# Kernel tuning notes

Hardware: AMD Instinct MI355X
Metric: run time of the kernel (lower is better)

## Reference

```python
import jax, jax.numpy as jnp
import numpy as np

N, L, D = 512, 40, 128      # batch, peptide length, embedding dim
O, K, MHC = 256, 9, 34      # out_channels, kernel_size, mhc_len
STRIDE = 1


def setup_inputs() -> dict:
    key = jax.random.key(0)
    k1, k2, k3 = jax.random.split(key, 3)
    peptide_x = jax.random.normal(k1, (N, L, D), dtype=jnp.float32)
    mhc_x = jax.random.normal(k2, (N, MHC, D), dtype=jnp.float32)
    weight = jax.random.normal(k3, (O, K, MHC), dtype=jnp.float32) * 0.02  # truncated_normal std=0.02 approx
    bias = jnp.zeros((O,), dtype=jnp.float32)
    return {"peptide_x": peptide_x, "mhc_x": mhc_x, "weight": weight, "bias": bias}


def reference(peptide_x, mhc_x, weight, bias):
    # Per-sample dynamic kernel generation: [n, O, d, K]
    kernel = jax.nn.relu(jnp.einsum('nld,okl->nodk', mhc_x, weight))
    k = weight.shape[1]
    T = (peptide_x.shape[1] - k) // STRIDE + 1  # conv1d output length
    # Sliding windows of the peptide: [n, T, K, d]
    idx = jnp.arange(T)[:, None] * STRIDE + jnp.arange(k)[None, :]
    win = peptide_x[:, idx, :]
    # Grouped (groups=batch) conv1d as a batched contraction: [n, O, T]
    out = jnp.einsum('ntkd,nodk->not', win, kernel) + bias[None, :, None]
    return out
```

## Files before the change

kernel.cpp:

```cpp
#include <hip/hip_runtime.h>
#include <hip/hip_bf16.h>

typedef unsigned short u16;
typedef unsigned int u32;
typedef __bf16 bf16x8 __attribute__((ext_vector_type(8)));
typedef float f32x4 __attribute__((ext_vector_type(4)));
typedef unsigned int u32x4 __attribute__((ext_vector_type(4)));
typedef unsigned int u32x2 __attribute__((ext_vector_type(2)));

#define NN 512
#define LL 40
#define DD 128
#define OO 256
#define KK 9
#define MHCL 34
#define TT 32
#define PSTR 136
#define KDSTR 72
#define WPADL 64

#define PEPT_U16 (LL * PSTR)
#define KS_U16   (32 * KDSTR)

__device__ __forceinline__ u16 f2bf(float x) {
    unsigned int u = __builtin_bit_cast(unsigned int, x);
    u = (u + 0x7FFFu + ((u >> 16) & 1u)) >> 16;
    return (u16)u;
}
__device__ __forceinline__ u32 pk2(float a, float b) {
    __hip_bfloat162 h = __float22bfloat162_rn(make_float2(a, b));
    u32 r;
    __builtin_memcpy(&r, &h, 4);
    return r;
}
__device__ __forceinline__ bf16x8 lds_read8(const u16* p) {
    u32x4 r;
    __builtin_memcpy(&r, __builtin_assume_aligned(p, 16), 16);
    return __builtin_bit_cast(bf16x8, r);
}
__device__ __forceinline__ f32x4 mfma16(bf16x8 a, bf16x8 b, f32x4 c) {
    return __builtin_amdgcn_mfma_f32_16x16x32_bf16(a, b, c, 0, 0, 0);
}

__global__ void w_convert(const float* __restrict__ wgt, u32* __restrict__ wp) {
    int i = blockIdx.x * 256 + threadIdx.x;
    if (i >= OO * KK * (WPADL / 2)) return;
    int o = i / (KK * (WPADL / 2));
    int r = i - o * (KK * (WPADL / 2));
    int k = r >> 5;
    int lp = (r & 31) << 1;
    const float* src = wgt + ((size_t)o * KK + k) * MHCL;
    float a = (lp     < MHCL) ? src[lp]     : 0.f;
    float b = (lp + 1 < MHCL) ? src[lp + 1] : 0.f;
    wp[i] = pk2(a, b);
}

template<bool PRE>
__global__ __launch_bounds__(256, 2)
void iconv_kernel(const float* __restrict__ pept,
                  const float* __restrict__ mhc,
                  const float* __restrict__ wgt,
                  const u16* __restrict__ wp,
                  const float* __restrict__ bias,
                  float* __restrict__ out)
{
    __shared__ __align__(16) u16 s_mem[PEPT_U16 + 4 * KS_U16];

    const int tid  = threadIdx.x;
    const int wave = tid >> 6;
    const int pair = wave >> 1;
    const int dh   = wave & 1;
    const int lane = tid & 63;
    const int quad = lane >> 4;
    const int l16  = lane & 15;

    const int n  = blockIdx.x >> 2;
    const int oq = blockIdx.x & 3;
    const int obase = (oq * 2 + pair) * 32;

    u16* const s_pept = s_mem;
    u16* const ks     = s_mem + PEPT_U16 + wave * KS_U16;

    auto loadW = [&](int o_base, int k, bf16x8 wF[2][2]) {
        if (PRE) {
            #pragma unroll
            for (int mt = 0; mt < 2; ++mt) {
                const u16* wr = wp + ((size_t)(o_base + mt * 16 + l16) * KK + k) * WPADL;
                u32x4 r0, r1;
                __builtin_memcpy(&r0, __builtin_assume_aligned(wr + quad * 8, 16), 16);
                __builtin_memcpy(&r1, __builtin_assume_aligned(wr + 32 + quad * 8, 16), 16);
                wF[mt][0] = __builtin_bit_cast(bf16x8, r0);
                wF[mt][1] = __builtin_bit_cast(bf16x8, r1);
            }
        } else {
            #pragma unroll
            for (int mt = 0; mt < 2; ++mt) {
                const float* wrow = wgt + ((size_t)(o_base + mt * 16 + l16) * KK + k) * MHCL;
                float w8[8];
                __builtin_memcpy(w8, __builtin_assume_aligned(wrow + quad * 8, 8), 32);
                u16 h0[8];
                #pragma unroll
                for (int j = 0; j < 8; ++j) h0[j] = f2bf(w8[j]);
                __builtin_memcpy(&wF[mt][0], h0, 16);
                u16 h1[8] = {0,0,0,0,0,0,0,0};
                if (quad == 0) { h1[0] = f2bf(wrow[32]); h1[1] = f2bf(wrow[33]); }
                __builtin_memcpy(&wF[mt][1], h1, 16);
            }
        }
    };

    bf16x8 wB[2][2];
    loadW(obase, 0, wB);

    bf16x8 mA[4][2];
    {
        const float* mg = mhc + (size_t)n * MHCL * DD;
        #pragma unroll
        for (int di = 0; di < 4; ++di) {
            const int d = dh * 64 + di * 16 + l16;
            u16 h0[8];
            #pragma unroll
            for (int j = 0; j < 8; ++j)
                h0[j] = f2bf(mg[(size_t)(quad * 8 + j) * DD + d]);
            __builtin_memcpy(&mA[di][0], h0, 16);
            u16 h1[8] = {0,0,0,0,0,0,0,0};
            if (quad == 0) {
                h1[0] = f2bf(mg[(size_t)32 * DD + d]);
                h1[1] = f2bf(mg[(size_t)33 * DD + d]);
            }
            __builtin_memcpy(&mA[di][1], h1, 16);
        }
    }

    {
        const float* pg = pept + (size_t)n * LL * DD;
        #pragma unroll 1
        for (int i = tid; i < (LL * DD) / 4; i += 256) {
            int row = i >> 5, c4 = (i & 31) << 2;
            f32x4 v;
            __builtin_memcpy(&v, __builtin_assume_aligned(pg + row * DD + c4, 16), 16);
            u32x2 h = { pk2(v[0], v[1]), pk2(v[2], v[3]) };
            __builtin_memcpy(__builtin_assume_aligned(&s_pept[row * PSTR + c4], 8), &h, 8);
        }
    }
    __syncthreads();

    f32x4 acc00 = {0.f,0.f,0.f,0.f}, acc01 = acc00, acc10 = acc00, acc11 = acc00;

    #pragma unroll 3
    for (int k = 0; k < KK; ++k) {
        #pragma unroll
        for (int di = 0; di < 4; ++di) {
            f32x4 c0 = {0.f,0.f,0.f,0.f}, c1 = c0;
            c0 = mfma16(mA[di][0], wB[0][0], c0);
            c0 = mfma16(mA[di][1], wB[0][1], c0);
            c1 = mfma16(mA[di][0], wB[1][0], c1);
            c1 = mfma16(mA[di][1], wB[1][1], c1);
            u32x2 p0 = { pk2(fmaxf(c0[0], 0.f), fmaxf(c0[1], 0.f)),
                         pk2(fmaxf(c0[2], 0.f), fmaxf(c0[3], 0.f)) };
            u32x2 p1 = { pk2(fmaxf(c1[0], 0.f), fmaxf(c1[1], 0.f)),
                         pk2(fmaxf(c1[2], 0.f), fmaxf(c1[3], 0.f)) };
            __builtin_memcpy(__builtin_assume_aligned(&ks[l16 * KDSTR + di * 16 + quad * 4], 8), &p0, 8);
            __builtin_memcpy(__builtin_assume_aligned(&ks[(16 + l16) * KDSTR + di * 16 + quad * 4], 8), &p1, 8);
        }
        if (k < KK - 1) loadW(obase, k + 1, wB);
        #pragma unroll
        for (int ds = 0; ds < 2; ++ds) {
            bf16x8 kb0 = lds_read8(&ks[l16 * KDSTR + ds * 32 + quad * 8]);
            bf16x8 kb1 = lds_read8(&ks[(16 + l16) * KDSTR + ds * 32 + quad * 8]);
            bf16x8 ap0 = lds_read8(&s_pept[(k + l16) * PSTR + dh * 64 + ds * 32 + quad * 8]);
            bf16x8 ap1 = lds_read8(&s_pept[(k + 16 + l16) * PSTR + dh * 64 + ds * 32 + quad * 8]);
            acc00 = mfma16(ap0, kb0, acc00);
            acc01 = mfma16(ap0, kb1, acc01);
            acc10 = mfma16(ap1, kb0, acc10);
            acc11 = mfma16(ap1, kb1, acc11);
        }
    }

    if (dh == 1) {
        float* ox = (float*)ks;
        const int fb = lane * 16;
        __builtin_memcpy(__builtin_assume_aligned(&ox[fb +  0], 16), &acc00, 16);
        __builtin_memcpy(__builtin_assume_aligned(&ox[fb +  4], 16), &acc01, 16);
        __builtin_memcpy(__builtin_assume_aligned(&ox[fb +  8], 16), &acc10, 16);
        __builtin_memcpy(__builtin_assume_aligned(&ox[fb + 12], 16), &acc11, 16);
    }
    __syncthreads();
    if (dh == 0) {
        const float* px = (const float*)(s_mem + PEPT_U16 + (wave + 1) * KS_U16);
        const int fb = lane * 16;
        f32x4 q00, q01, q10, q11;
        __builtin_memcpy(&q00, __builtin_assume_aligned(&px[fb +  0], 16), 16);
        __builtin_memcpy(&q01, __builtin_assume_aligned(&px[fb +  4], 16), 16);
        __builtin_memcpy(&q10, __builtin_assume_aligned(&px[fb +  8], 16), 16);
        __builtin_memcpy(&q11, __builtin_assume_aligned(&px[fb + 12], 16), 16);
        const float bv0 = bias[obase + l16];
        const float bv1 = bias[obase + 16 + l16];
        f32x4 r00 = acc00 + q00 + bv0;
        f32x4 r01 = acc01 + q01 + bv1;
        f32x4 r10 = acc10 + q10 + bv0;
        f32x4 r11 = acc11 + q11 + bv1;
        float* ob = out + ((size_t)n * OO + obase) * TT;
        __builtin_memcpy(__builtin_assume_aligned(ob + (size_t)l16 * TT + quad * 4, 16), &r00, 16);
        __builtin_memcpy(__builtin_assume_aligned(ob + (size_t)(16 + l16) * TT + quad * 4, 16), &r01, 16);
        __builtin_memcpy(__builtin_assume_aligned(ob + (size_t)l16 * TT + 16 + quad * 4, 16), &r10, 16);
        __builtin_memcpy(__builtin_assume_aligned(ob + (size_t)(16 + l16) * TT + 16 + quad * 4, 16), &r11, 16);
    }
}

extern "C" void kernel_launch(void* const* d_in, const int* in_sizes, int n_in,
                              void* d_out, int out_size, void* d_ws, size_t ws_size,
                              hipStream_t stream) {
    const float* pept = (const float*)d_in[0];
    const float* mhc  = (const float*)d_in[1];
    const float* wgt  = (const float*)d_in[2];
    const float* bias = (const float*)d_in[3];
    float* out = (float*)d_out;

    const size_t w_bytes = (size_t)OO * KK * WPADL * sizeof(u16);
    if (ws_size >= w_bytes) {
        w_convert<<<dim3((OO * KK * (WPADL / 2) + 255) / 256), dim3(256), 0, stream>>>(wgt, (u32*)d_ws);
        iconv_kernel<true><<<dim3(NN * 4), dim3(256), 0, stream>>>(pept, mhc, wgt, (const u16*)d_ws, bias, out);
    } else {
        iconv_kernel<false><<<dim3(NN * 4), dim3(256), 0, stream>>>(pept, mhc, wgt, nullptr, bias, out);
    }
}
```

Before: 116.6 us.

## Pre-convert peptide to bf16 in workspace and read it directly from global

Adds a separate kernel that converts the whole peptide tensor to bf16 in the workspace. The main kernel then reads peptide fragments straight from global memory instead of staging them in LDS. This drops the peptide LDS buffer and the __syncthreads before the main loop, shrinking shared memory so the launch bound can rise to 6 blocks per CU. In exchange it adds an extra kernel launch and a full pass over the peptide. The main loop also now issues global loads, whose latency may be harder to hide than LDS reads.

```diff
diff --git a/kernel.cpp b/kernel.cpp
--- a/kernel.cpp
+++ b/kernel.cpp
@@ -33,7 +33,7 @@
     __builtin_memcpy(&r, &h, 4);
     return r;
 }
-__device__ __forceinline__ bf16x8 lds_read8(const u16* p) {
+__device__ __forceinline__ bf16x8 ld8(const u16* p) {
     u32x4 r;
     __builtin_memcpy(&r, __builtin_assume_aligned(p, 16), 16);
     return __builtin_bit_cast(bf16x8, r);
@@ -55,16 +55,20 @@
     wp[i] = pk2(a, b);
 }
 
-template<bool PRE>
-__global__ __launch_bounds__(256, 2)
-void iconv_kernel(const float* __restrict__ pept,
-                  const float* __restrict__ mhc,
-                  const float* __restrict__ wgt,
-                  const u16* __restrict__ wp,
-                  const float* __restrict__ bias,
-                  float* __restrict__ out)
+__global__ void p_convert(const float* __restrict__ pept, u32* __restrict__ pp) {
+    size_t i = (size_t)blockIdx.x * 256 + threadIdx.x;
+    if (i >= (size_t)NN * LL * DD / 2) return;
+    pp[i] = pk2(pept[2 * i], pept[2 * i + 1]);
+}
+
+__global__ __launch_bounds__(256, 6)
+void iconv_fast(const float* __restrict__ mhc,
+                const u16* __restrict__ wp,
+                const u16* __restrict__ pb,
+                const float* __restrict__ bias,
+                float* __restrict__ out)
 {
-    __shared__ __align__(16) u16 s_mem[PEPT_U16 + 4 * KS_U16];
+    __shared__ __align__(16) u16 s_ks[4 * KS_U16];
 
     const int tid  = threadIdx.x;
     const int wave = tid >> 6;
@@ -78,34 +82,17 @@
     const int oq = blockIdx.x & 3;
     const int obase = (oq * 2 + pair) * 32;
 
-    u16* const s_pept = s_mem;
-    u16* const ks     = s_mem + PEPT_U16 + wave * KS_U16;
+    u16* const ks = s_ks + wave * KS_U16;
 
     auto loadW = [&](int o_base, int k, bf16x8 wF[2][2]) {
-        if (PRE) {
-            #pragma unroll
-            for (int mt = 0; mt < 2; ++mt) {
-                const u16* wr = wp + ((size_t)(o_base + mt * 16 + l16) * KK + k) * WPADL;
-                u32x4 r0, r1;
-                __builtin_memcpy(&r0, __builtin_assume_aligned(wr + quad * 8, 16), 16);
-                __builtin_memcpy(&r1, __builtin_assume_aligned(wr + 32 + quad * 8, 16), 16);
-                wF[mt][0] = __builtin_bit_cast(bf16x8, r0);
-                wF[mt][1] = __builtin_bit_cast(bf16x8, r1);
-            }
-        } else {
-            #pragma unroll
-            for (int mt = 0; mt < 2; ++mt) {
-                const float* wrow = wgt + ((size_t)(o_base + mt * 16 + l16) * KK + k) * MHCL;
-                float w8[8];
-                __builtin_memcpy(w8, __builtin_assume_aligned(wrow + quad * 8, 8), 32);
-                u16 h0[8];
-                #pragma unroll
-                for (int j = 0; j < 8; ++j) h0[j] = f2bf(w8[j]);
-                __builtin_memcpy(&wF[mt][0], h0, 16);
-                u16 h1[8] = {0,0,0,0,0,0,0,0};
-                if (quad == 0) { h1[0] = f2bf(wrow[32]); h1[1] = f2bf(wrow[33]); }
-                __builtin_memcpy(&wF[mt][1], h1, 16);
-            }
+        #pragma unroll
+        for (int mt = 0; mt < 2; ++mt) {
+            const u16* wr = wp + ((size_t)(o_base + mt * 16 + l16) * KK + k) * WPADL;
+            u32x4 r0, r1;
+            __builtin_memcpy(&r0, __builtin_assume_aligned(wr + quad * 8, 16), 16);
+            __builtin_memcpy(&r1, __builtin_assume_aligned(wr + 32 + quad * 8, 16), 16);
+            wF[mt][0] = __builtin_bit_cast(bf16x8, r0);
+            wF[mt][1] = __builtin_bit_cast(bf16x8, r1);
         }
     };
 
@@ -132,18 +119,7 @@
         }
     }
 
-    {
-        const float* pg = pept + (size_t)n * LL * DD;
-        #pragma unroll 1
-        for (int i = tid; i < (LL * DD) / 4; i += 256) {
-            int row = i >> 5, c4 = (i & 31) << 2;
-            f32x4 v;
-            __builtin_memcpy(&v, __builtin_assume_aligned(pg + row * DD + c4, 16), 16);
-            u32x2 h = { pk2(v[0], v[1]), pk2(v[2], v[3]) };
-            __builtin_memcpy(__builtin_assume_aligned(&s_pept[row * PSTR + c4], 8), &h, 8);
-        }
-    }
-    __syncthreads();
+    const u16* const pr = pb + (size_t)n * LL * DD;
 
     f32x4 acc00 = {0.f,0.f,0.f,0.f}, acc01 = acc00, acc10 = acc00, acc11 = acc00;
 
@@ -166,10 +142,146 @@
         if (k < KK - 1) loadW(obase, k + 1, wB);
         #pragma unroll
         for (int ds = 0; ds < 2; ++ds) {
-            bf16x8 kb0 = lds_read8(&ks[l16 * KDSTR + ds * 32 + quad * 8]);
-            bf16x8 kb1 = lds_read8(&ks[(16 + l16) * KDSTR + ds * 32 + quad * 8]);
-            bf16x8 ap0 = lds_read8(&s_pept[(k + l16) * PSTR + dh * 64 + ds * 32 + quad * 8]);
-            bf16x8 ap1 = lds_read8(&s_pept[(k + 16 + l16) * PSTR + dh * 64 + ds * 32 + quad * 8]);
+            bf16x8 kb0 = ld8(&ks[l16 * KDSTR + ds * 32 + quad * 8]);
+            bf16x8 kb1 = ld8(&ks[(16 + l16) * KDSTR + ds * 32 + quad * 8]);
+            bf16x8 ap0 = ld8(&pr[(size_t)(k + l16) * DD + dh * 64 + ds * 32 + quad * 8]);
+            bf16x8 ap1 = ld8(&pr[(size_t)(k + 16 + l16) * DD + dh * 64 + ds * 32 + quad * 8]);
+            acc00 = mfma16(ap0, kb0, acc00);
+            acc01 = mfma16(ap0, kb1, acc01);
+            acc10 = mfma16(ap1, kb0, acc10);
+            acc11 = mfma16(ap1, kb1, acc11);
+        }
+    }
+
+    if (dh == 1) {
+        float* ox = (float*)ks;
+        const int fb = lane * 16;
+        __builtin_memcpy(__builtin_assume_aligned(&ox[fb +  0], 16), &acc00, 16);
+        __builtin_memcpy(__builtin_assume_aligned(&ox[fb +  4], 16), &acc01, 16);
+        __builtin_memcpy(__builtin_assume_aligned(&ox[fb +  8], 16), &acc10, 16);
+        __builtin_memcpy(__builtin_assume_aligned(&ox[fb + 12], 16), &acc11, 16);
+    }
+    __syncthreads();
+    if (dh == 0) {
+        const float* px = (const float*)(s_ks + (wave + 1) * KS_U16);
+        const int fb = lane * 16;
+        f32x4 q00, q01, q10, q11;
+        __builtin_memcpy(&q00, __builtin_assume_aligned(&px[fb +  0], 16), 16);
+        __builtin_memcpy(&q01, __builtin_assume_aligned(&px[fb +  4], 16), 16);
+        __builtin_memcpy(&q10, __builtin_assume_aligned(&px[fb +  8], 16), 16);
+        __builtin_memcpy(&q11, __builtin_assume_aligned(&px[fb + 12], 16), 16);
+        const float bv0 = bias[obase + l16];
+        const float bv1 = bias[obase + 16 + l16];
+        f32x4 r00 = acc00 + q00 + bv0;
+        f32x4 r01 = acc01 + q01 + bv1;
+        f32x4 r10 = acc10 + q10 + bv0;
+        f32x4 r11 = acc11 + q11 + bv1;
+        float* ob = out + ((size_t)n * OO + obase) * TT;
+        __builtin_memcpy(__builtin_assume_aligned(ob + (size_t)l16 * TT + quad * 4, 16), &r00, 16);
+        __builtin_memcpy(__builtin_assume_aligned(ob + (size_t)(16 + l16) * TT + quad * 4, 16), &r01, 16);
+        __builtin_memcpy(__builtin_assume_aligned(ob + (size_t)l16 * TT + 16 + quad * 4, 16), &r10, 16);
+        __builtin_memcpy(__builtin_assume_aligned(ob + (size_t)(16 + l16) * TT + 16 + quad * 4, 16), &r11, 16);
+    }
+}
+
+__global__ __launch_bounds__(256, 2)
+void iconv_ref(const float* __restrict__ pept,
+               const float* __restrict__ mhc,
+               const float* __restrict__ wgt,
+               const float* __restrict__ bias,
+               float* __restrict__ out)
+{
+    __shared__ __align__(16) u16 s_mem[PEPT_U16 + 4 * KS_U16];
+    const int tid  = threadIdx.x;
+    const int wave = tid >> 6;
+    const int pair = wave >> 1;
+    const int dh   = wave & 1;
+    const int lane = tid & 63;
+    const int quad = lane >> 4;
+    const int l16  = lane & 15;
+    const int n  = blockIdx.x >> 2;
+    const int oq = blockIdx.x & 3;
+    const int obase = (oq * 2 + pair) * 32;
+    u16* const s_pept = s_mem;
+    u16* const ks     = s_mem + PEPT_U16 + wave * KS_U16;
+
+    auto loadW = [&](int o_base, int k, bf16x8 wF[2][2]) {
+        #pragma unroll
+        for (int mt = 0; mt < 2; ++mt) {
+            const float* wrow = wgt + ((size_t)(o_base + mt * 16 + l16) * KK + k) * MHCL;
+            float w8[8];
+            __builtin_memcpy(w8, __builtin_assume_aligned(wrow + quad * 8, 8), 32);
+            u16 h0[8];
+            #pragma unroll
+            for (int j = 0; j < 8; ++j) h0[j] = f2bf(w8[j]);
+            __builtin_memcpy(&wF[mt][0], h0, 16);
+            u16 h1[8] = {0,0,0,0,0,0,0,0};
+            if (quad == 0) { h1[0] = f2bf(wrow[32]); h1[1] = f2bf(wrow[33]); }
+            __builtin_memcpy(&wF[mt][1], h1, 16);
+        }
+    };
+
+    bf16x8 wB[2][2];
+    loadW(obase, 0, wB);
+
+    bf16x8 mA[4][2];
+    {
+        const float* mg = mhc + (size_t)n * MHCL * DD;
+        #pragma unroll
+        for (int di = 0; di < 4; ++di) {
+            const int d = dh * 64 + di * 16 + l16;
+            u16 h0[8];
+            #pragma unroll
+            for (int j = 0; j < 8; ++j)
+                h0[j] = f2bf(mg[(size_t)(quad * 8 + j) * DD + d]);
+            __builtin_memcpy(&mA[di][0], h0, 16);
+            u16 h1[8] = {0,0,0,0,0,0,0,0};
+            if (quad == 0) {
+                h1[0] = f2bf(mg[(size_t)32 * DD + d]);
+                h1[1] = f2bf(mg[(size_t)33 * DD + d]);
+            }
+            __builtin_memcpy(&mA[di][1], h1, 16);
+        }
+    }
+
+    {
+        const float* pg = pept + (size_t)n * LL * DD;
+        #pragma unroll 1
+        for (int i = tid; i < (LL * DD) / 4; i += 256) {
+            int row = i >> 5, c4 = (i & 31) << 2;
+            f32x4 v;
+            __builtin_memcpy(&v, __builtin_assume_aligned(pg + row * DD + c4, 16), 16);
+            u32x2 h = { pk2(v[0], v[1]), pk2(v[2], v[3]) };
+            __builtin_memcpy(__builtin_assume_aligned(&s_pept[row * PSTR + c4], 8), &h, 8);
+        }
+    }
+    __syncthreads();
+
+    f32x4 acc00 = {0.f,0.f,0.f,0.f}, acc01 = acc00, acc10 = acc00, acc11 = acc00;
+
+    #pragma unroll 3
+    for (int k = 0; k < KK; ++k) {
+        #pragma unroll
+        for (int di = 0; di < 4; ++di) {
+            f32x4 c0 = {0.f,0.f,0.f,0.f}, c1 = c0;
+            c0 = mfma16(mA[di][0], wB[0][0], c0);
+            c0 = mfma16(mA[di][1], wB[0][1], c0);
+            c1 = mfma16(mA[di][0], wB[1][0], c1);
+            c1 = mfma16(mA[di][1], wB[1][1], c1);
+            u32x2 p0 = { pk2(fmaxf(c0[0], 0.f), fmaxf(c0[1], 0.f)),
+                         pk2(fmaxf(c0[2], 0.f), fmaxf(c0[3], 0.f)) };
+            u32x2 p1 = { pk2(fmaxf(c1[0], 0.f), fmaxf(c1[1], 0.f)),
+                         pk2(fmaxf(c1[2], 0.f), fmaxf(c1[3], 0.f)) };
+            __builtin_memcpy(__builtin_assume_aligned(&ks[l16 * KDSTR + di * 16 + quad * 4], 8), &p0, 8);
+            __builtin_memcpy(__builtin_assume_aligned(&ks[(16 + l16) * KDSTR + di * 16 + quad * 4], 8), &p1, 8);
+        }
+        if (k < KK - 1) loadW(obase, k + 1, wB);
+        #pragma unroll
+        for (int ds = 0; ds < 2; ++ds) {
+            bf16x8 kb0 = ld8(&ks[l16 * KDSTR + ds * 32 + quad * 8]);
+            bf16x8 kb1 = ld8(&ks[(16 + l16) * KDSTR + ds * 32 + quad * 8]);
+            bf16x8 ap0 = ld8(&s_pept[(k + l16) * PSTR + dh * 64 + ds * 32 + quad * 8]);
+            bf16x8 ap1 = ld8(&s_pept[(k + 16 + l16) * PSTR + dh * 64 + ds * 32 + quad * 8]);
             acc00 = mfma16(ap0, kb0, acc00);
             acc01 = mfma16(ap0, kb1, acc01);
             acc10 = mfma16(ap1, kb0, acc10);
@@ -218,10 +330,14 @@
     float* out = (float*)d_out;
 
     const size_t w_bytes = (size_t)OO * KK * WPADL * sizeof(u16);
-    if (ws_size >= w_bytes) {
-        w_convert<<<dim3((OO * KK * (WPADL / 2) + 255) / 256), dim3(256), 0, stream>>>(wgt, (u32*)d_ws);
-        iconv_kernel<true><<<dim3(NN * 4), dim3(256), 0, stream>>>(pept, mhc, wgt, (const u16*)d_ws, bias, out);
+    const size_t p_bytes = (size_t)NN * LL * DD * sizeof(u16);
+    if (ws_size >= w_bytes + p_bytes) {
+        u16* wp = (u16*)d_ws;
+        u16* pp = (u16*)((char*)d_ws + w_bytes);
+        w_convert<<<dim3((OO * KK * (WPADL / 2) + 255) / 256), dim3(256), 0, stream>>>(wgt, (u32*)wp);
+        p_convert<<<dim3((NN * LL * DD / 2 + 255) / 256), dim3(256), 0, stream>>>(pept, (u32*)pp);
+        iconv_fast<<<dim3(NN * 4), dim3(256), 0, stream>>>(mhc, wp, pp, bias, out);
     } else {
-        iconv_kernel<false><<<dim3(NN * 4), dim3(256), 0, stream>>>(pept, mhc, wgt, nullptr, bias, out);
-    }
-}
+        iconv_ref<<<dim3(NN * 4), dim3(256), 0, stream>>>(pept, mhc, wgt, bias, out);
+    }
+}
```

Measured after the change: 202.1 us. 1.73x slower.
